# Performance work log

Hardware: AMD Instinct MI355X
Metric: run time of the kernel (lower is better)

The kernel has to match this reference:

```python
import jax, jax.numpy as jnp
import numpy as np

ENC_H = 512      # encoder_hidden_dim -> encoder_out feature = 2*ENC_H
DEC_H = 512      # decoder_hidden_dim
B, S = 32, 2048  # batch, max_seq_len


def setup_inputs() -> dict:
    key = jax.random.key(0)
    k1, k2, k3, k4, k5, k6, k7 = jax.random.split(key, 7)
    encoder_out = jax.random.normal(k1, (B, S, 2 * ENC_H), dtype=jnp.float32)
    hidden = jax.random.normal(k2, (B, DEC_H), dtype=jnp.float32)
    lengths = jax.random.randint(k3, (B,), 1, S + 1, dtype=jnp.int64)
    in_dim = 2 * ENC_H + DEC_H
    # torch nn.Linear default init scale
    attn_w = jax.random.uniform(k4, (DEC_H, in_dim), jnp.float32, -1.0, 1.0) / np.sqrt(in_dim)
    attn_b = jax.random.uniform(k5, (DEC_H,), jnp.float32, -1.0, 1.0) / np.sqrt(in_dim)
    v_w = jax.random.uniform(k6, (1, DEC_H), jnp.float32, -1.0, 1.0) / np.sqrt(DEC_H)
    v_b = jax.random.uniform(k7, (1,), jnp.float32, -1.0, 1.0) / np.sqrt(DEC_H)
    return {"encoder_out": encoder_out, "hidden": hidden, "lengths": lengths,
            "attn_w": attn_w, "attn_b": attn_b, "v_w": v_w, "v_b": v_b}


def reference(encoder_out, hidden, lengths, attn_w, attn_b, v_w, v_b):
    # encoder_out: [B,S,2E], hidden: [B,D], lengths: [B]
    Bc, Sc, _ = encoder_out.shape
    h = jnp.broadcast_to(hidden[:, None, :], (Bc, Sc, hidden.shape[-1]))
    temp = jnp.concatenate([h, encoder_out], axis=2)           # [B,S,D+2E]
    e = jnp.tanh(jnp.einsum('bsf,df->bsd', temp, attn_w) + attn_b)  # [B,S,D]
    scores = jnp.einsum('bsd,d->bs', e, v_w[0]) + v_b[0]       # [B,S]
    mask = jnp.arange(Sc)[None, :] < lengths[:, None]          # [B,S]
    scores = jnp.where(mask, scores, -jnp.inf)
    energy = jax.nn.softmax(scores, axis=1)                    # softmax over valid positions
    energy = jnp.where(mask, energy, 0.0)                      # padded positions stay exactly 0
    context = jnp.einsum('bs,bse->be', energy, encoder_out)    # [B,2E]
    return context
```

## Files before the change

### kernel.cpp

```cpp
#include <hip/hip_runtime.h>
#include <hip/hip_bf16.h>
#include <math.h>

typedef __attribute__((ext_vector_type(8))) short short8;
typedef __attribute__((ext_vector_type(4))) unsigned uint4v;
typedef __attribute__((ext_vector_type(16))) float f32x16;

static constexpr int B  = 32;
static constexpr int S  = 2048;
static constexpr int D  = 512;
static constexpr int KE = 1024;
static constexpr int IN = 1536;

__device__ __forceinline__ unsigned pk2(float lo, float hi) {
    __hip_bfloat162 t = __float22bfloat162_rn(make_float2(lo, hi));
    unsigned u;
    __builtin_memcpy(&u, &t, 4);
    return u;
}

__device__ __forceinline__ short8 pack8(float4 f0, float4 f1) {
    uint4v u;
    u[0] = pk2(f0.x, f0.y);
    u[1] = pk2(f0.z, f0.w);
    u[2] = pk2(f1.x, f1.y);
    u[3] = pk2(f1.z, f1.w);
    short8 r;
    __builtin_memcpy(&r, &u, 16);
    return r;
}

__device__ __forceinline__ float tanh_fast(float x) {
    float e = __expf(2.0f * x);
    return (e - 1.0f) * __builtin_amdgcn_rcpf(e + 1.0f);
}

__global__ void k_prep(const float* __restrict__ attn_w,
                       const float* __restrict__ hidden,
                       const float* __restrict__ attn_b,
                       unsigned short* __restrict__ Bf,
                       float* __restrict__ u) {
    if (blockIdx.x < 256) {
        int o = blockIdx.x * 256 + threadIdx.x;
        int l6  = o & 63;
        int grp = o >> 6;
        int d = (grp & 15) * 32 + (l6 & 31);
        int k = (grp >> 4) * 16 + (l6 >> 5) * 8;
        const float* src = attn_w + (size_t)d * IN + 512 + k;
        float4 f0 = *(const float4*)src;
        float4 f1 = *(const float4*)(src + 4);
        ((short8*)Bf)[o] = pack8(f0, f1);
    } else {
        int gid = (blockIdx.x - 256) * 256 + threadIdx.x;
        int b = gid >> 9;
        int d = gid & (D - 1);
        const float* h = hidden + b * D;
        const float* w = attn_w + (size_t)d * IN;
        float acc = attn_b[d];
        for (int k = 0; k < D; k += 4) {
            float4 hv = *(const float4*)(h + k);
            float4 wv = *(const float4*)(w + k);
            acc += hv.x * wv.x + hv.y * wv.y + hv.z * wv.z + hv.w * wv.w;
        }
        u[gid] = acc;
    }
}

#define LOADA(K, DST) do {                                     \
    const float* _p0 = a0p + (K) * 16;                         \
    const float* _p1 = a1p + (K) * 16;                         \
    DST[0][0] = *(const float4*)_p0;                           \
    DST[0][1] = *(const float4*)(_p0 + 4);                     \
    DST[1][0] = *(const float4*)_p1;                           \
    DST[1][1] = *(const float4*)(_p1 + 4);                     \
} while (0)

#define LOADB(K, DST) do {                                     \
    _Pragma("unroll")                                          \
    for (int _jt = 0; _jt < 4; _jt++)                          \
        DST[_jt] = bb[(size_t)(K) * 1024 + _jt * 64];          \
} while (0)

__global__ __launch_bounds__(256, 2) void k_scores(
    const float* __restrict__ enc, const unsigned short* __restrict__ Bfrag,
    const float* __restrict__ u, const float* __restrict__ v_w,
    const float* __restrict__ v_b, const int* __restrict__ lengths,
    float* __restrict__ scores)
{
    __shared__ float sPart[4][64];

    const int b   = blockIdx.y;
    const int s0  = blockIdx.x * 64;
    const int len = lengths[b];
    if (s0 >= len) return;

    const int tid = threadIdx.x;
    const int w   = tid >> 6;
    const int l   = tid & 63;

    const float* a0p = enc + ((size_t)b * S + s0 + (l & 31)) * KE + ((l >> 5) << 3);
    const float* a1p = a0p + (size_t)32 * KE;
    const short8* bb = (const short8*)Bfrag + (w * 4) * 64 + l;

    f32x16 acc[2][4];
    #pragma unroll
    for (int mt = 0; mt < 2; mt++)
        #pragma unroll
        for (int jt = 0; jt < 4; jt++)
            #pragma unroll
            for (int e = 0; e < 16; e++) acc[mt][jt][e] = 0.f;

    float4 pa[4][2][2];
    short8 pb[2][4];
    LOADA(0, pa[0]);
    LOADA(1, pa[1]);
    LOADA(2, pa[2]);
    LOADA(3, pa[3]);
    LOADB(0, pb[0]);
    LOADB(1, pb[1]);

    #pragma unroll 4
    for (int k16 = 0; k16 < 64; ++k16) {
        const int st = k16 & 3;
        const int bp = k16 & 1;
        short8 a0 = pack8(pa[st][0][0], pa[st][0][1]);
        short8 a1 = pack8(pa[st][1][0], pa[st][1][1]);
        LOADA((k16 + 4) & 63, pa[st]);
        #pragma unroll
        for (int jt = 0; jt < 4; jt++) {
            acc[0][jt] = __builtin_amdgcn_mfma_f32_32x32x16_bf16(a0, pb[bp][jt], acc[0][jt], 0, 0, 0);
            acc[1][jt] = __builtin_amdgcn_mfma_f32_32x32x16_bf16(a1, pb[bp][jt], acc[1][jt], 0, 0, 0);
        }
        LOADB((k16 + 2) & 63, pb[bp]);
    }

    float vv[4], uu[4];
    const float* ub = u + b * D;
    #pragma unroll
    for (int jt = 0; jt < 4; jt++) {
        int d = w * 128 + jt * 32 + (l & 31);
        vv[jt] = v_w[d];
        uu[jt] = ub[d];
    }
    float red[2][16];
    #pragma unroll
    for (int mt = 0; mt < 2; mt++)
        #pragma unroll
        for (int r = 0; r < 16; r++) {
            float s = 0.f;
            #pragma unroll
            for (int jt = 0; jt < 4; jt++)
                s += vv[jt] * tanh_fast(acc[mt][jt][r] + uu[jt]);
            red[mt][r] = s;
        }
    #pragma unroll
    for (int off = 16; off >= 1; off >>= 1)
        #pragma unroll
        for (int mt = 0; mt < 2; mt++)
            #pragma unroll
            for (int r = 0; r < 16; r++)
                red[mt][r] += __shfl_xor(red[mt][r], off);
    if ((l & 31) == 0) {
        int hb = (l >> 5) * 4;
        #pragma unroll
        for (int mt = 0; mt < 2; mt++)
            #pragma unroll
            for (int r = 0; r < 16; r++)
                sPart[w][mt * 32 + (r & 3) + 8 * (r >> 2) + hb] = red[mt][r];
    }
    __syncthreads();
    if (tid < 64)
        scores[b * S + s0 + tid] =
            sPart[0][tid] + sPart[1][tid] + sPart[2][tid] + sPart[3][tid] + v_b[0];
}

__global__ void k_softmax(const float* __restrict__ scores,
                          const int* __restrict__ lengths,
                          float* __restrict__ energy) {
    const int b = blockIdx.x;
    const int len = lengths[b];
    const int tid = threadIdx.x;
    const int lane = tid & 63, wave = tid >> 6;
    __shared__ float red[4];
    const float* sc = scores + b * S;

    float m = -INFINITY;
    for (int s = tid; s < len; s += 256) m = fmaxf(m, sc[s]);
    #pragma unroll
    for (int off = 32; off >= 1; off >>= 1) m = fmaxf(m, __shfl_xor(m, off));
    if (lane == 0) red[wave] = m;
    __syncthreads();
    m = fmaxf(fmaxf(red[0], red[1]), fmaxf(red[2], red[3]));
    __syncthreads();

    float sum = 0.f;
    for (int s = tid; s < len; s += 256) sum += __expf(sc[s] - m);
    #pragma unroll
    for (int off = 32; off >= 1; off >>= 1) sum += __shfl_xor(sum, off);
    if (lane == 0) red[wave] = sum;
    __syncthreads();
    float inv = 1.f / (red[0] + red[1] + red[2] + red[3]);

    for (int s = tid; s < len; s += 256) energy[b * S + s] = __expf(sc[s] - m) * inv;
}

__global__ void k_context(const float* __restrict__ enc,
                          const float* __restrict__ energy,
                          const int* __restrict__ lengths,
                          float* __restrict__ out) {
    const int b = blockIdx.y;
    const int len = lengths[b];
    const int s0 = blockIdx.x * 128;
    if (s0 >= len) return;
    const int s1 = min(s0 + 128, len);
    const int tid = threadIdx.x;
    const float4* encb = (const float4*)(enc + (size_t)b * S * KE);
    const float* en = energy + b * S;
    float4 acc[8];
    #pragma unroll
    for (int i = 0; i < 8; i++) acc[i] = make_float4(0.f, 0.f, 0.f, 0.f);
    int s = s0;
    for (; s + 8 <= s1; s += 8) {
        #pragma unroll
        for (int i = 0; i < 8; i++) {
            float wgt = en[s + i];
            float4 v = encb[(size_t)(s + i) * 256 + tid];
            acc[i].x += wgt * v.x; acc[i].y += wgt * v.y;
            acc[i].z += wgt * v.z; acc[i].w += wgt * v.w;
        }
    }
    for (; s < s1; s++) {
        float wgt = en[s];
        float4 v = encb[(size_t)s * 256 + tid];
        acc[0].x += wgt * v.x; acc[0].y += wgt * v.y;
        acc[0].z += wgt * v.z; acc[0].w += wgt * v.w;
    }
    #pragma unroll
    for (int i = 1; i < 8; i++) {
        acc[0].x += acc[i].x; acc[0].y += acc[i].y;
        acc[0].z += acc[i].z; acc[0].w += acc[i].w;
    }
    float* o = out + b * KE + tid * 4;
    atomicAdd(o + 0, acc[0].x);
    atomicAdd(o + 1, acc[0].y);
    atomicAdd(o + 2, acc[0].z);
    atomicAdd(o + 3, acc[0].w);
}

extern "C" void kernel_launch(void* const* d_in, const int* in_sizes, int n_in,
                              void* d_out, int out_size, void* d_ws, size_t ws_size,
                              hipStream_t stream) {
    const float* enc    = (const float*)d_in[0];
    const float* hidden = (const float*)d_in[1];
    const int*   lengths= (const int*)d_in[2];
    const float* attn_w = (const float*)d_in[3];
    const float* attn_b = (const float*)d_in[4];
    const float* v_w    = (const float*)d_in[5];
    const float* v_b    = (const float*)d_in[6];
    float* out = (float*)d_out;

    float* ws     = (float*)d_ws;
    float* u      = ws;
    float* scores = u + B * D;
    float* energy = scores + B * S;
    unsigned short* Bf = (unsigned short*)(energy + B * S);

    (void)hipMemsetAsync(d_out, 0, (size_t)out_size * sizeof(float), stream);
    k_prep  <<<dim3(320), 256, 0, stream>>>(attn_w, hidden, attn_b, Bf, u);
    k_scores<<<dim3(S / 64, B), 256, 0, stream>>>(enc, Bf, u, v_w, v_b, lengths, scores);
    k_softmax<<<dim3(B), 256, 0, stream>>>(scores, lengths, energy);
    k_context<<<dim3(16, B), 256, 0, stream>>>(enc, energy, lengths, out);
}
```

Before: 525.8 us.

## Stage encoder tiles through LDS as bf16 instead of per-wave global loads

Before this change, each of the four waves loaded the full 64-row encoder A tile from global memory and converted it to bf16 on its own, so every block read the same data four times. The new code has the whole block load each 64x64 K-chunk once, pack it to bf16, and store it in a double-buffered LDS array padded to 19 short4 per row against bank conflicts. Waves then read their MFMA A fragments from LDS, which cuts global and L2 traffic by about four times. The cost is two __syncthreads per chunk, extra LDS use that may reduce occupancy, and a shallower register prefetch pipeline.

After: 454.7 us. 1.16x faster.

```diff
diff --git a/kernel.cpp b/kernel.cpp
--- a/kernel.cpp
+++ b/kernel.cpp
@@ -2,8 +2,8 @@
 #include <hip/hip_bf16.h>
 #include <math.h>
 
+typedef __attribute__((ext_vector_type(4))) short short4v;
 typedef __attribute__((ext_vector_type(8))) short short8;
-typedef __attribute__((ext_vector_type(4))) unsigned uint4v;
 typedef __attribute__((ext_vector_type(16))) float f32x16;
 
 static constexpr int B  = 32;
@@ -19,14 +19,24 @@
     return u;
 }
 
+__device__ __forceinline__ short4v pack4(float4 f) {
+    unsigned u2[2] = { pk2(f.x, f.y), pk2(f.z, f.w) };
+    short4v r;
+    __builtin_memcpy(&r, u2, 8);
+    return r;
+}
+
 __device__ __forceinline__ short8 pack8(float4 f0, float4 f1) {
-    uint4v u;
-    u[0] = pk2(f0.x, f0.y);
-    u[1] = pk2(f0.z, f0.w);
-    u[2] = pk2(f1.x, f1.y);
-    u[3] = pk2(f1.z, f1.w);
+    unsigned u[4] = { pk2(f0.x, f0.y), pk2(f0.z, f0.w), pk2(f1.x, f1.y), pk2(f1.z, f1.w) };
     short8 r;
-    __builtin_memcpy(&r, &u, 16);
+    __builtin_memcpy(&r, u, 16);
+    return r;
+}
+
+__device__ __forceinline__ short8 cat44(short4v lo, short4v hi) {
+    short8 r;
+    __builtin_memcpy(&r, &lo, 8);
+    __builtin_memcpy(((char*)&r) + 8, &hi, 8);
     return r;
 }
 
@@ -66,15 +76,6 @@
     }
 }
 
-#define LOADA(K, DST) do {                                     \
-    const float* _p0 = a0p + (K) * 16;                         \
-    const float* _p1 = a1p + (K) * 16;                         \
-    DST[0][0] = *(const float4*)_p0;                           \
-    DST[0][1] = *(const float4*)(_p0 + 4);                     \
-    DST[1][0] = *(const float4*)_p1;                           \
-    DST[1][1] = *(const float4*)(_p1 + 4);                     \
-} while (0)
-
 #define LOADB(K, DST) do {                                     \
     _Pragma("unroll")                                          \
     for (int _jt = 0; _jt < 4; _jt++)                          \
@@ -87,6 +88,7 @@
     const float* __restrict__ v_b, const int* __restrict__ lengths,
     float* __restrict__ scores)
 {
+    __shared__ short4v ldsA[2][64 * 19];
     __shared__ float sPart[4][64];
 
     const int b   = blockIdx.y;
@@ -98,8 +100,12 @@
     const int w   = tid >> 6;
     const int l   = tid & 63;
 
-    const float* a0p = enc + ((size_t)b * S + s0 + (l & 31)) * KE + ((l >> 5) << 3);
-    const float* a1p = a0p + (size_t)32 * KE;
+    const float* encb = enc + ((size_t)b * S + s0) * KE;
+    const int mr = tid >> 4;
+    const int cw = tid & 15;
+    const float* aG = encb + (size_t)mr * KE + cw * 4;
+    const int wbase = mr * 19 + cw;
+
     const short8* bb = (const short8*)Bfrag + (w * 4) * 64 + l;
 
     f32x16 acc[2][4];
@@ -110,28 +116,48 @@
             #pragma unroll
             for (int e = 0; e < 16; e++) acc[mt][jt][e] = 0.f;
 
-    float4 pa[4][2][2];
     short8 pb[2][4];
-    LOADA(0, pa[0]);
-    LOADA(1, pa[1]);
-    LOADA(2, pa[2]);
-    LOADA(3, pa[3]);
     LOADB(0, pb[0]);
     LOADB(1, pb[1]);
 
-    #pragma unroll 4
-    for (int k16 = 0; k16 < 64; ++k16) {
-        const int st = k16 & 3;
-        const int bp = k16 & 1;
-        short8 a0 = pack8(pa[st][0][0], pa[st][0][1]);
-        short8 a1 = pack8(pa[st][1][0], pa[st][1][1]);
-        LOADA((k16 + 4) & 63, pa[st]);
-        #pragma unroll
-        for (int jt = 0; jt < 4; jt++) {
-            acc[0][jt] = __builtin_amdgcn_mfma_f32_32x32x16_bf16(a0, pb[bp][jt], acc[0][jt], 0, 0, 0);
-            acc[1][jt] = __builtin_amdgcn_mfma_f32_32x32x16_bf16(a1, pb[bp][jt], acc[1][jt], 0, 0, 0);
-        }
-        LOADB((k16 + 2) & 63, pb[bp]);
+    {
+        float4 g[4];
+        #pragma unroll
+        for (int i = 0; i < 4; i++) g[i] = *(const float4*)(aG + (size_t)i * 16 * KE);
+        #pragma unroll
+        for (int i = 0; i < 4; i++) ldsA[0][wbase + i * 16 * 19] = pack4(g[i]);
+    }
+    __syncthreads();
+
+    const int rb0 = (l & 31) * 19 + (l >> 5) * 2;
+    const int rb1 = rb0 + 32 * 19;
+
+    #pragma unroll 1
+    for (int c = 0; c < 16; ++c) {
+        const int buf = c & 1;
+        const int cn  = (c + 1) & 15;
+        float4 g[4];
+        #pragma unroll
+        for (int i = 0; i < 4; i++)
+            g[i] = *(const float4*)(aG + (size_t)i * 16 * KE + cn * 64);
+        #pragma unroll
+        for (int t2 = 0; t2 < 4; ++t2) {
+            const short4v* base = &ldsA[buf][t2 * 4];
+            short8 a0 = cat44(base[rb0], base[rb0 + 1]);
+            short8 a1 = cat44(base[rb1], base[rb1 + 1]);
+            const int bp = t2 & 1;
+            #pragma unroll
+            for (int jt = 0; jt < 4; jt++) {
+                acc[0][jt] = __builtin_amdgcn_mfma_f32_32x32x16_bf16(a0, pb[bp][jt], acc[0][jt], 0, 0, 0);
+                acc[1][jt] = __builtin_amdgcn_mfma_f32_32x32x16_bf16(a1, pb[bp][jt], acc[1][jt], 0, 0, 0);
+            }
+            LOADB((c * 4 + t2 + 2) & 63, pb[bp]);
+        }
+        __syncthreads();
+        #pragma unroll
+        for (int i = 0; i < 4; i++)
+            ldsA[buf ^ 1][wbase + i * 16 * 19] = pack4(g[i]);
+        __syncthreads();
     }
 
     float vv[4], uu[4];
```
